# Kernel tuning notes

Hardware: AMD Instinct MI355X
Metric: run time of the kernel (lower is better)

Reference implementation:

```python
import jax, jax.numpy as jnp
import numpy as np

C = 32
N = 10000
E = 100000
LAT = 128
EPS = 1e-8
SQ3 = 3.0 ** 0.5
AVG_NEIGH = 10.0


def _sh2(p):
    # real l=2 spherical harmonics with principal axis = y (e3nn convention), m = -2..2
    x, y, z = p[..., 0], p[..., 1], p[..., 2]
    return jnp.stack([SQ3 * z * x, SQ3 * x * y, 0.5 * (3.0 * y * y - 1.0),
                      SQ3 * y * z, 0.5 * SQ3 * (z * z - x * x)], axis=-1)

# fixed sample points -> pseudoinverse for fitting Wigner-D at l=2: Y2(R p) = Y2(p) @ D2^T
_np_rng = np.random.default_rng(0)
_X = _np_rng.normal(size=(16, 3))
_X = _X / np.linalg.norm(_X, axis=1, keepdims=True)
_Xj = jnp.asarray(_X, jnp.float32)
_P2 = jnp.asarray(np.linalg.pinv(np.asarray(_sh2(jnp.asarray(_X, jnp.float32)))), jnp.float32)


def _wigner(vec):
    # per-edge rotation R with R @ n = e_y (edge aligned to y axis, e3nn convention)
    n = vec / jnp.clip(jnp.linalg.norm(vec, axis=-1, keepdims=True), 1e-9)
    ex = jnp.array([1.0, 0.0, 0.0], n.dtype)
    ez = jnp.array([0.0, 0.0, 1.0], n.dtype)
    a = jnp.where(jnp.abs(n[:, :1]) < 0.9, ex, ez)
    u = a - jnp.sum(a * n, axis=-1, keepdims=True) * n
    u = u / jnp.clip(jnp.linalg.norm(u, axis=-1, keepdims=True), 1e-9)
    v = jnp.cross(u, n)
    D1 = jnp.stack([u, n, v], axis=1)  # (E,3,3); Wigner-D for l=1 in (x,y,z) basis
    pts = jnp.einsum('eij,kj->eki', D1, _Xj)  # rotated sample points (E,K,3)
    D2 = jnp.swapaxes(jnp.einsum('mk,ekn->emn', _P2, _sh2(pts)), 1, 2)  # (E,5,5)
    return D1, D2


def _split(x):
    # flat [C x 0e | C x 1e | C x 2e] -> (.,C), (.,C,3), (.,C,5)
    return x[:, :C], x[:, C:4 * C].reshape(-1, C, 3), x[:, 4 * C:].reshape(-1, C, 5)


def _sln(x0, x1, x2, g0, b0, g1, g2):
    # separable layer norm: LN on scalars, degree-balanced RMS on l>0
    mu = jnp.mean(x0, axis=-1, keepdims=True)
    var = jnp.mean((x0 - mu) ** 2, axis=-1, keepdims=True)
    x0 = (x0 - mu) * jax.lax.rsqrt(var + EPS) * g0 + b0
    v = 0.5 * (jnp.mean(x1 ** 2, axis=(1, 2)) + jnp.mean(x2 ** 2, axis=(1, 2)))
    s = jax.lax.rsqrt(v + EPS)[:, None, None]
    return x0, x1 * s * g1[None, :, None], x2 * s * g2[None, :, None]


def _forward(latents, node_features, edge_features, edge_vector,
             g0n, b0n, g1n, g2n, g0e, b0e, g1e, g2e,
             w0s, w01, w02, wr1_1, wi1_1, wr1_2, wi1_2, wr2_2, wi2_2,
             wp0, bp0, wp1, wp2, w_env, b_env,
             atom_type, edge_index, active_edges):
    n0, n1, n2 = _sln(*_split(node_features), g0n, b0n, g1n, g2n)
    e0, e1, e2 = _sln(*_split(edge_features), g0e, b0e, g1e, g2e)
    ctr = edge_index[0][active_edges]
    nbr = edge_index[1][active_edges]
    vec = edge_vector[active_edges]
    lat = latents[active_edges]
    D1, D2 = _wigner(vec)
    # gather + concat: center | edge | neighbor, 3C channels per degree
    x0 = jnp.concatenate([n0[ctr], e0[active_edges], n0[nbr]], axis=1)
    x1 = jnp.concatenate([n1[ctr], e1[active_edges], n1[nbr]], axis=1)
    x2 = jnp.concatenate([n2[ctr], e2[active_edges], n2[nbr]], axis=1)
    # rotate into edge frame
    x1 = jnp.einsum('emn,ecn->ecm', D1, x1)
    x2 = jnp.einsum('emn,ecn->ecm', D2, x2)
    # SO2 linear (block structure over m about the edge axis = y; m index = l+m)
    s0 = 1.0 / jnp.sqrt(jnp.float32(9 * C))
    s1 = 1.0 / jnp.sqrt(jnp.float32(6 * C))
    s2 = 1.0 / jnp.sqrt(jnp.float32(3 * C))
    in0 = jnp.concatenate([x0, x1[:, :, 1], x2[:, :, 2]], axis=1)  # (E,9C) m=0
    y0 = in0 @ w0s.T * s0      # (E,3C): C scalars + 2C gates
    y1_0 = in0 @ w01.T * s0
    y2_0 = in0 @ w02.T * s0
    xp1 = jnp.concatenate([x1[:, :, 2], x2[:, :, 3]], axis=1)  # m=+1
    xm1 = jnp.concatenate([x1[:, :, 0], x2[:, :, 1]], axis=1)  # m=-1
    y1_p = (xp1 @ wr1_1.T - xm1 @ wi1_1.T) * s1
    y1_m = (xp1 @ wi1_1.T + xm1 @ wr1_1.T) * s1
    y2_p1 = (xp1 @ wr1_2.T - xm1 @ wi1_2.T) * s1
    y2_m1 = (xp1 @ wi1_2.T + xm1 @ wr1_2.T) * s1
    xp2 = x2[:, :, 4]
    xm2 = x2[:, :, 0]
    y2_p2 = (xp2 @ wr2_2.T - xm2 @ wi2_2.T) * s2
    y2_m2 = (xp2 @ wi2_2.T + xm2 @ wr2_2.T) * s2
    y1 = jnp.stack([y1_m, y1_0, y1_p], axis=-1)                      # (E,C,3)
    y2 = jnp.stack([y2_m2, y2_m1, y2_0, y2_p1, y2_p2], axis=-1)      # (E,C,5)
    # rotate back to global frame
    y1 = jnp.einsum('enm,ecn->ecm', D1, y1)
    y2 = jnp.einsum('enm,ecn->ecm', D2, y2)
    # Gate activation
    scal = jax.nn.silu(y0[:, :C])
    gate1 = jax.nn.sigmoid(y0[:, C:2 * C])
    gate2 = jax.nn.sigmoid(y0[:, 2 * C:])
    m1 = y1 * gate1[:, :, None]
    m2 = y2 * gate2[:, :, None]
    # lin_post (e3nn Linear, per-degree, bias on scalars)
    sc = 1.0 / jnp.sqrt(jnp.float32(C))
    m0 = scal @ wp0.T * sc + bp0
    m1 = jnp.einsum('dc,ecm->edm', wp1, m1) * sc
    m2 = jnp.einsum('dc,ecm->edm', wp2, m2) * sc
    # env weighting: per-irrep elementwise scalars from latents
    w = lat @ w_env.T * (1.0 / jnp.sqrt(jnp.float32(LAT))) + b_env
    m0 = m0 * w[:, :C]
    m1 = m1 * w[:, C:2 * C][:, :, None]
    m2 = m2 * w[:, 2 * C:][:, :, None]
    msg = jnp.concatenate([m0, m1.reshape(-1, 3 * C), m2.reshape(-1, 5 * C)], axis=1)
    agg = jax.ops.segment_sum(msg, ctr, num_segments=N) * (1.0 / jnp.sqrt(AVG_NEIGH))
    # residual update with logit-0 coefficient
    cu = 0.5
    c_old = 1.0 / jnp.sqrt(1.0 + cu * cu)
    c_new = cu * c_old
    return c_old * node_features + c_new * agg


def setup_inputs() -> dict:
    key = jax.random.key(0)
    ks = jax.random.split(key, 32)
    f = lambda i, shape: jax.random.normal(ks[i], shape, dtype=jnp.float32)
    return {
        'latents': f(0, (E, LAT)),
        'node_features': f(1, (N, 9 * C)),
        'edge_features': f(2, (E, 9 * C)),
        'edge_vector': f(3, (E, 3)),
        'atom_type': jax.random.randint(ks[4], (N,), 0, 10),
        'edge_index': jax.random.randint(ks[5], (2, E), 0, N),
        'active_edges': jnp.arange(E),
        'g0n': 1.0 + 0.1 * f(6, (C,)), 'b0n': 0.1 * f(7, (C,)),
        'g1n': 1.0 + 0.1 * f(8, (C,)), 'g2n': 1.0 + 0.1 * f(9, (C,)),
        'g0e': 1.0 + 0.1 * f(10, (C,)), 'b0e': 0.1 * f(11, (C,)),
        'g1e': 1.0 + 0.1 * f(12, (C,)), 'g2e': 1.0 + 0.1 * f(13, (C,)),
        'w0s': f(14, (3 * C, 9 * C)), 'w01': f(15, (C, 9 * C)), 'w02': f(16, (C, 9 * C)),
        'wr1_1': f(17, (C, 6 * C)), 'wi1_1': f(18, (C, 6 * C)),
        'wr1_2': f(19, (C, 6 * C)), 'wi1_2': f(20, (C, 6 * C)),
        'wr2_2': f(21, (C, 3 * C)), 'wi2_2': f(22, (C, 3 * C)),
        'wp0': f(23, (C, C)), 'bp0': 0.1 * f(24, (C,)),
        'wp1': f(25, (C, C)), 'wp2': f(26, (C, C)),
        'w_env': f(27, (3 * C, LAT)), 'b_env': 1.0 + 0.1 * f(28, (3 * C,)),
    }


def reference(latents, node_features, edge_features, edge_vector,
              g0n, b0n, g1n, g2n, g0e, b0e, g1e, g2e,
              w0s, w01, w02, wr1_1, wi1_1, wr1_2, wi1_2, wr2_2, wi2_2,
              wp0, bp0, wp1, wp2, w_env, b_env,
              atom_type, edge_index, active_edges):
    return _forward(latents, node_features, edge_features, edge_vector,
                    g0n, b0n, g1n, g2n, g0e, b0e, g1e, g2e,
                    w0s, w01, w02, wr1_1, wi1_1, wr1_2, wi1_2, wr2_2, wi2_2,
                    wp0, bp0, wp1, wp2, w_env, b_env,
                    atom_type, edge_index, active_edges)
```

## Files before the change

### kernel.cpp

```cpp
#include <hip/hip_runtime.h>
#include <hip/hip_bf16.h>
#include <math.h>

#define NN 10000
#define EE 100000
#define EPB 16
#define AST 1000
#define YSTH 456
#define PSTA 40
#define PSTP 36
#define MST 296
#define STG0 10368

#define SEG0 0
#define SEGP1 288
#define SEGM1 480
#define SEGP2 672
#define SEGM2 768
#define SEGL 864

#define Y0o   0
#define Y10o  96
#define Y20o  128
#define Y1Po  160
#define Y1Mo  192
#define Y2P1o 224
#define Y2M1o 256
#define Y2P2o 288
#define Y2M2o 320
#define WENVo 352

#define PK1 0
#define PK2 46080
#define PK3 95232
#define PK4 107520
#define PKP 119808
#define PKTOT 122880

#define WS_NRM 0
#define WS_PK  11520000
#define WS_CNT 11765760
#define WS_OFF 11831296
#define WS_CUR 11896832
#define WS_EL  11962368
#define WS_MSG 12486656
#define WS_REQ (WS_MSG + (size_t)EE*288*2)

#define SQ3F  1.7320508075688772f
#define S0F   0.05892556509887896f
#define S1F   0.07216878364870323f
#define S2F   0.10206207261596575f
#define SEF   0.08838834764831845f
#define SCF   0.17677669529663687f
#define COLDF 0.8944271909999159f
#define COEFF 0.1414213562373095f

typedef __attribute__((ext_vector_type(8))) short bf16x8;
typedef __attribute__((ext_vector_type(4))) float f32x4;

__device__ __forceinline__ ushort f2bf(float f) {
    __hip_bfloat16 h = __float2bfloat16(f);
    return __builtin_bit_cast(unsigned short, h);
}
__device__ __forceinline__ float bf2f(ushort u) {
    union { unsigned u; float f; } v; v.u = (unsigned)u << 16; return v.f;
}
__device__ __forceinline__ float fsig(float x) {
    return __builtin_amdgcn_rcpf(1.f + __expf(-x));
}

__device__ __forceinline__ int planar(int k) {
    if (k < 32) return k;
    if (k < 128) { int c = (k - 32) / 3, m = (k - 32) % 3; return 32 + 32*m + c; }
    int c = (k - 128) / 5, m = (k - 128) % 5; return 128 + 32*m + c;
}

__global__ __launch_bounds__(256) void pack_k(
    const float* __restrict__ w0s, const float* __restrict__ w01, const float* __restrict__ w02,
    const float* __restrict__ wr11, const float* __restrict__ wi11,
    const float* __restrict__ wr12, const float* __restrict__ wi12,
    const float* __restrict__ wr22, const float* __restrict__ wi22,
    const float* __restrict__ wenv,
    const float* __restrict__ wp0, const float* __restrict__ wp1, const float* __restrict__ wp2,
    ushort* __restrict__ pk)
{
    int i = blockIdx.x * 256 + threadIdx.x;
    if (i >= PKTOT) return;
    float val;
    if (i < PK2) {
        int idx = i - PK1;
        int tile = idx / 4608, rem = idx % 4608;
        int chunk = rem / 512, rem2 = rem % 512;
        int lane = rem2 / 8, j = rem2 % 8;
        int col = tile * 16 + (lane & 15);
        int k = chunk * 32 + (lane >> 4) * 8 + j;
        if (col < 96)       val = w0s[col * 288 + k];
        else if (col < 128) val = w01[(col - 96) * 288 + k];
        else                val = w02[(col - 128) * 288 + k];
    } else if (i < PK3) {
        int idx = i - PK2;
        int tile = idx / 6144, rem = idx % 6144;
        int chunk = rem / 512, rem2 = rem % 512;
        int lane = rem2 / 8, j = rem2 % 8;
        int col = tile * 16 + (lane & 15);
        int k = chunk * 32 + (lane >> 4) * 8 + j;
        int grp = col >> 5, c = col & 31;
        if (k < 192) {
            val = (grp == 0) ? wr11[c*192 + k] : (grp == 1) ? wi11[c*192 + k]
                : (grp == 2) ? wr12[c*192 + k] : wi12[c*192 + k];
        } else {
            int kk = k - 192;
            val = (grp == 0) ? -wi11[c*192 + kk] : (grp == 1) ? wr11[c*192 + kk]
                : (grp == 2) ? -wi12[c*192 + kk] : wr12[c*192 + kk];
        }
    } else if (i < PK4) {
        int idx = i - PK3;
        int tile = idx / 3072, rem = idx % 3072;
        int chunk = rem / 512, rem2 = rem % 512;
        int lane = rem2 / 8, j = rem2 % 8;
        int col = tile * 16 + (lane & 15);
        int k = chunk * 32 + (lane >> 4) * 8 + j;
        int grp = col >> 5, c = col & 31;
        if (k < 96) val = grp ? wi22[c*96 + k] : wr22[c*96 + k];
        else        val = grp ? wr22[c*96 + k - 96] : -wi22[c*96 + k - 96];
    } else if (i < PKP) {
        int idx = i - PK4;
        int tile = idx / 2048, rem = idx % 2048;
        int chunk = rem / 512, rem2 = rem % 512;
        int lane = rem2 / 8, j = rem2 % 8;
        int col = tile * 16 + (lane & 15);
        int k = chunk * 32 + (lane >> 4) * 8 + j;
        val = wenv[col * 128 + k];
    } else {
        int idx = i - PKP;
        int wpi = idx / 1024, rem = idx % 1024;
        int ct = rem / 512, rem2 = rem % 512;
        int lane = rem2 / 8, j = rem2 % 8;
        int col = ct * 16 + (lane & 15);
        int k = (lane >> 4) * 8 + j;
        const float* w = (wpi == 0) ? wp0 : (wpi == 1) ? wp1 : wp2;
        val = w[col * 32 + k];
    }
    pk[i] = f2bf(val);
}

__global__ __launch_bounds__(256) void node_norm_k(
    const float* __restrict__ nf,
    const float* __restrict__ g0, const float* __restrict__ b0,
    const float* __restrict__ g1, const float* __restrict__ g2,
    float* __restrict__ nrm, float* __restrict__ out)
{
    int row = blockIdx.x * 4 + (threadIdx.x >> 6);
    if (row >= NN) return;
    int lane = threadIdx.x & 63;
    const float* r = nf + (size_t)row * 288;
    float v0 = r[lane];
    float v1 = r[lane + 64];
    float v2 = r[lane + 128];
    float v3 = r[lane + 192];
    float v4 = (lane < 32) ? r[lane + 256] : 0.f;
    float s0 = 0.f, s0q = 0.f, q1 = 0.f, q2 = 0.f;
    if (lane < 32) { s0 = v0; s0q = v0*v0; } else { q1 = v0*v0; }
    q1 += v1*v1;
    q2 += v2*v2 + v3*v3 + v4*v4;
#pragma unroll
    for (int m = 1; m < 64; m <<= 1) {
        s0  += __shfl_xor(s0, m);
        s0q += __shfl_xor(s0q, m);
        q1  += __shfl_xor(q1, m);
        q2  += __shfl_xor(q2, m);
    }
    float mu  = s0 * (1.f/32.f);
    float var = s0q * (1.f/32.f) - mu*mu;
    float rs0 = rsqrtf(var + 1e-8f);
    float rv  = 0.5f * (q1 * (1.f/96.f) + q2 * (1.f/160.f));
    float rs  = rsqrtf(rv + 1e-8f);
    float* nr = nrm + (size_t)row * 288;
    {
        float res;
        if (lane < 32) res = (v0 - mu) * rs0 * g0[lane] + b0[lane];
        else { int c = (lane - 32) / 3; res = v0 * rs * g1[c]; }
        nr[planar(lane)] = res;
    }
    { int k = lane + 64;  int c = (k - 32) / 3;  nr[planar(k)] = v1 * rs * g1[c]; }
    { int k = lane + 128; int c = (k - 128) / 5; nr[planar(k)] = v2 * rs * g2[c]; }
    { int k = lane + 192; int c = (k - 128) / 5; nr[planar(k)] = v3 * rs * g2[c]; }
    if (lane < 32) { int k = lane + 256; int c = (k - 128) / 5; nr[planar(k)] = v4 * rs * g2[c]; }
    if (out) {
        float* orow = out + (size_t)row * 288;
        orow[lane]       = COLDF * v0;
        orow[lane + 64]  = COLDF * v1;
        orow[lane + 128] = COLDF * v2;
        orow[lane + 192] = COLDF * v3;
        if (lane < 32) orow[lane + 256] = COLDF * v4;
    }
}

__global__ __launch_bounds__(256) void zero_k(int* __restrict__ counts) {
    int i = blockIdx.x * 256 + threadIdx.x;
    if (i < NN) counts[i] = 0;
}
__global__ __launch_bounds__(256) void hist_k(
    const int* __restrict__ eidx, const int* __restrict__ act, int* __restrict__ counts) {
    int e = blockIdx.x * 256 + threadIdx.x;
    if (e >= EE) return;
    atomicAdd(&counts[eidx[act[e]]], 1);
}
__global__ __launch_bounds__(256) void scan_k(
    const int* __restrict__ counts, int* __restrict__ offs, int* __restrict__ curs) {
    __shared__ int sbuf[256];
    __shared__ int scarry;
    if (threadIdx.x == 0) scarry = 0;
    __syncthreads();
    for (int base = 0; base < NN; base += 256) {
        int i = base + threadIdx.x;
        int v = (i < NN) ? counts[i] : 0;
        sbuf[threadIdx.x] = v;
        __syncthreads();
        for (int off = 1; off < 256; off <<= 1) {
            int t = (threadIdx.x >= off) ? sbuf[threadIdx.x - off] : 0;
            __syncthreads();
            sbuf[threadIdx.x] += t;
            __syncthreads();
        }
        int excl = sbuf[threadIdx.x] - v;
        if (i < NN) { int o = scarry + excl; offs[i] = o; curs[i] = o; }
        __syncthreads();
        if (threadIdx.x == 255) scarry += sbuf[255];
        __syncthreads();
    }
}
__global__ __launch_bounds__(256) void scatter_k(
    const int* __restrict__ eidx, const int* __restrict__ act,
    int* __restrict__ curs, int* __restrict__ eslot) {
    int e = blockIdx.x * 256 + threadIdx.x;
    if (e >= EE) return;
    int pos = atomicAdd(&curs[eidx[act[e]]], 1);
    eslot[e] = pos;
}

__global__ __launch_bounds__(256) void gather_k(
    const ushort* __restrict__ msg, const int* __restrict__ offs,
    const int* __restrict__ counts,
    const float* __restrict__ nf, float* __restrict__ out)
{
    int node = blockIdx.x * 4 + (threadIdx.x >> 6);
    if (node >= NN) return;
    int lane = threadIdx.x & 63;
    int start = offs[node], cnt = counts[node];
    float a0 = 0.f, a1 = 0.f, a2 = 0.f, a3 = 0.f, a4 = 0.f;
    const ushort* mr = msg + (size_t)start * 288;
    for (int i = 0; i < cnt; ++i, mr += 288) {
        a0 += bf2f(mr[lane]);
        a1 += bf2f(mr[lane + 64]);
        a2 += bf2f(mr[lane + 128]);
        a3 += bf2f(mr[lane + 192]);
        if (lane < 32) a4 += bf2f(mr[lane + 256]);
    }
    const float* r = nf + (size_t)node * 288;
    float* o = out + (size_t)node * 288;
    o[lane]       = COLDF * r[lane]       + COEFF * a0;
    o[lane + 64]  = COLDF * r[lane + 64]  + COEFF * a1;
    o[lane + 128] = COLDF * r[lane + 128] + COEFF * a2;
    o[lane + 192] = COLDF * r[lane + 192] + COEFF * a3;
    if (lane < 32) o[lane + 256] = COLDF * r[lane + 256] + COEFF * a4;
}

__global__ __launch_bounds__(512, 6) void edge_k(
    const float* __restrict__ lat, const float* __restrict__ ef,
    const float* __restrict__ evec,
    const int* __restrict__ eidx, const int* __restrict__ act,
    const int* __restrict__ eslot,
    const float* __restrict__ g0e, const float* __restrict__ b0e,
    const float* __restrict__ g1e, const float* __restrict__ g2e,
    const ushort* __restrict__ pk,
    const float* __restrict__ bp0, const float* __restrict__ benv,
    const float* __restrict__ nrm, ushort* __restrict__ msg, float* __restrict__ out)
{
    __shared__ __align__(16) ushort sA[EPB * AST];
    __shared__ __align__(16) ushort sY[EPB * YSTH];
    __shared__ float sD1[EPB][12];
    __shared__ float sD2[EPB][28];
    __shared__ int sAe[EPB], sCtr[EPB], sNbr[EPB], sSlot[EPB];

    const int tid = threadIdx.x;
    const int wv = tid >> 6, lane = tid & 63;

    if (tid < EPB) {
        int ae = act[blockIdx.x * EPB + tid];
        sAe[tid] = ae;
        sCtr[tid] = eidx[ae];
        sNbr[tid] = eidx[EE + ae];
        sSlot[tid] = eslot ? eslot[blockIdx.x * EPB + tid] : 0;

        float vx = evec[3*ae], vy = evec[3*ae+1], vz = evec[3*ae+2];
        float nnv = fmaxf(sqrtf(vx*vx + vy*vy + vz*vz), 1e-9f);
        float nx = vx/nnv, ny = vy/nnv, nz = vz/nnv;
        float ax, az;
        if (fabsf(nx) < 0.9f) { ax = 1.f; az = 0.f; } else { ax = 0.f; az = 1.f; }
        float adn = ax*nx + az*nz;
        float ux = ax - adn*nx, uy = -adn*ny, uz = az - adn*nz;
        float un = fmaxf(sqrtf(ux*ux + uy*uy + uz*uz), 1e-9f);
        ux /= un; uy /= un; uz /= un;
        float wx = uy*nz - uz*ny, wy = uz*nx - ux*nz, wz = ux*ny - uy*nx;

        sD1[tid][0] = ux; sD1[tid][1] = uy; sD1[tid][2] = uz;
        sD1[tid][3] = nx; sD1[tid][4] = ny; sD1[tid][5] = nz;
        sD1[tid][6] = wx; sD1[tid][7] = wy; sD1[tid][8] = wz;

        float d2[5][5];
        d2[0][0] = wz*ux + uz*wx;  d2[0][1] = wx*uy + ux*wy;  d2[0][2] = SQ3F*wy*uy;
        d2[0][3] = wy*uz + uy*wz;  d2[0][4] = wz*uz - wx*ux;
        d2[1][0] = uz*nx + nz*ux;  d2[1][1] = ux*ny + nx*uy;  d2[1][2] = SQ3F*uy*ny;
        d2[1][3] = uy*nz + ny*uz;  d2[1][4] = uz*nz - ux*nx;
        d2[2][0] = SQ3F*nz*nx;     d2[2][1] = SQ3F*nx*ny;     d2[2][2] = 1.5f*ny*ny - 0.5f;
        d2[2][3] = SQ3F*ny*nz;     d2[2][4] = 0.5f*SQ3F*(nz*nz - nx*nx);
        d2[3][0] = nz*wx + wz*nx;  d2[3][1] = nx*wy + wx*ny;  d2[3][2] = SQ3F*ny*wy;
        d2[3][3] = ny*wz + wy*nz;  d2[3][4] = nz*wz - nx*wx;
        d2[4][0] = wz*wx - uz*ux;  d2[4][1] = wx*wy - ux*uy;  d2[4][2] = 0.5f*SQ3F*(wy*wy - uy*uy);
        d2[4][3] = wy*wz - uy*uz;  d2[4][4] = 0.5f*(wz*wz - uz*uz - wx*wx + ux*ux);
#pragma unroll
        for (int n = 0; n < 5; ++n)
#pragma unroll
            for (int m = 0; m < 5; ++m) sD2[tid][5*n + m] = d2[n][m];
    }
    __syncthreads();

    for (int it = 0; it < 2; ++it) {
        const int e = it * 8 + wv;
        const int ae = sAe[e];
        const int ctr = sCtr[e], nbr = sNbr[e];
        ushort* row = sA + e * AST;
        ushort* sEb = sY + e * YSTH;
        const float* efr = ef + (size_t)ae * 288;

        float ev0 = efr[lane];
        float ev1 = efr[lane + 64];
        float ev2 = efr[lane + 128];
        float ev3 = efr[lane + 192];
        float ev4 = (lane < 32) ? efr[lane + 256] : 0.f;
        float s0 = 0.f, s0q = 0.f, q1 = 0.f, q2 = 0.f;
        if (lane < 32) { s0 = ev0; s0q = ev0*ev0; } else { q1 = ev0*ev0; }
        q1 += ev1*ev1;
        q2 += ev2*ev2 + ev3*ev3 + ev4*ev4;
#pragma unroll
        for (int m = 1; m < 64; m <<= 1) {
            s0  += __shfl_xor(s0, m);
            s0q += __shfl_xor(s0q, m);
            q1  += __shfl_xor(q1, m);
            q2  += __shfl_xor(q2, m);
        }
        float mu  = s0 * (1.f/32.f);
        float rs0 = rsqrtf(s0q*(1.f/32.f) - mu*mu + 1e-8f);
        float rs  = rsqrtf(0.5f*(q1*(1.f/96.f) + q2*(1.f/160.f)) + 1e-8f);

        if (lane >= 32) { int c = (lane-32)/3, m = (lane-32)%3; sEb[32 + 32*m + c] = f2bf(ev0 * rs * g1e[c]); }
        { int k = lane+64;  int c = (k-32)/3,  m = (k-32)%3;  sEb[32 + 32*m + c]  = f2bf(ev1 * rs * g1e[c]); }
        { int k = lane+128; int c = (k-128)/5, m = (k-128)%5; sEb[128 + 32*m + c] = f2bf(ev2 * rs * g2e[c]); }
        { int k = lane+192; int c = (k-128)/5, m = (k-128)%5; sEb[128 + 32*m + c] = f2bf(ev3 * rs * g2e[c]); }
        if (lane < 32) { int k = lane+256; int c = (k-128)/5, m = (k-128)%5; sEb[128 + 32*m + c] = f2bf(ev4 * rs * g2e[c]); }

        if (lane < 32) {
            row[SEG0 + 32 + lane] = f2bf((ev0 - mu) * rs0 * g0e[lane] + b0e[lane]);
            row[SEG0 + lane]      = f2bf(nrm[(size_t)ctr*288 + lane]);
            row[SEG0 + 64 + lane] = f2bf(nrm[(size_t)nbr*288 + lane]);
        }
        {
            const float* lr = lat + (size_t)ae * 128;
            row[SEGL + lane]      = f2bf(lr[lane]);
            row[SEGL + 64 + lane] = f2bf(lr[lane + 64]);
        }
    }
    __syncthreads();

    {
        const int re = tid >> 5;
        const int rc = tid & 31;
        const float* bc = nrm + (size_t)sCtr[re] * 288;
        const float* bn = nrm + (size_t)sNbr[re] * 288;
        float c1v[3], c2v[5], n1v[3], n2v[5];
#pragma unroll
        for (int m = 0; m < 3; ++m) { c1v[m] = bc[32 + 32*m + rc]; n1v[m] = bn[32 + 32*m + rc]; }
#pragma unroll
        for (int m = 0; m < 5; ++m) { c2v[m] = bc[128 + 32*m + rc]; n2v[m] = bn[128 + 32*m + rc]; }
        float D1r[9], d2l[25];
#pragma unroll
        for (int i = 0; i < 9; ++i) D1r[i] = sD1[re][i];
#pragma unroll
        for (int i = 0; i < 25; ++i) d2l[i] = sD2[re][i];
        ushort* row = sA + re * AST;
        const ushort* sEb = sY + re * YSTH;
        float e1v[3], e2v[5];
#pragma unroll
        for (int m = 0; m < 3; ++m) e1v[m] = bf2f(sEb[32 + 32*m + rc]);
#pragma unroll
        for (int m = 0; m < 5; ++m) e2v[m] = bf2f(sEb[128 + 32*m + rc]);
#pragma unroll
        for (int p = 0; p < 3; ++p) {
            const int cc = rc + 32 * p;
            float x1v[3], x2v[5];
#pragma unroll
            for (int m = 0; m < 3; ++m) x1v[m] = (p == 0) ? c1v[m] : (p == 1) ? e1v[m] : n1v[m];
#pragma unroll
            for (int m = 0; m < 5; ++m) x2v[m] = (p == 0) ? c2v[m] : (p == 1) ? e2v[m] : n2v[m];
            float r0 = D1r[0]*x1v[0] + D1r[1]*x1v[1] + D1r[2]*x1v[2];
            float r1 = D1r[3]*x1v[0] + D1r[4]*x1v[1] + D1r[5]*x1v[2];
            float r2 = D1r[6]*x1v[0] + D1r[7]*x1v[1] + D1r[8]*x1v[2];
            float t[5];
#pragma unroll
            for (int m = 0; m < 5; ++m)
                t[m] = d2l[5*m+0]*x2v[0] + d2l[5*m+1]*x2v[1] + d2l[5*m+2]*x2v[2]
                     + d2l[5*m+3]*x2v[3] + d2l[5*m+4]*x2v[4];
            row[SEG0 + 96  + cc] = f2bf(r1);
            row[SEG0 + 192 + cc] = f2bf(t[2]);
            row[SEGP1 + cc]      = f2bf(r2);
            row[SEGP1 + 96 + cc] = f2bf(t[3]);
            row[SEGM1 + cc]      = f2bf(r0);
            row[SEGM1 + 96 + cc] = f2bf(t[1]);
            row[SEGP2 + cc]      = f2bf(t[4]);
            row[SEGM2 + cc]      = f2bf(t[0]);
        }
    }
    __syncthreads();

    for (int t = wv; t < 28; t += 8) {
        int kbase, nch, yoff, pbase; float scale;
        if (t < 10)      { kbase = SEG0;  nch = 9;  yoff = t*16;          scale = S0F; pbase = PK1 + t*9*512; }
        else if (t < 18) { kbase = SEGP1; nch = 12; yoff = 160+(t-10)*16; scale = S1F; pbase = PK2 + (t-10)*12*512; }
        else if (t < 22) { kbase = SEGP2; nch = 6;  yoff = 288+(t-18)*16; scale = S2F; pbase = PK3 + (t-18)*6*512; }
        else             { kbase = SEGL;  nch = 4;  yoff = 352+(t-22)*16; scale = SEF; pbase = PK4 + (t-22)*4*512; }
        f32x4 acc = {0.f, 0.f, 0.f, 0.f};
        const ushort* pa = sA + (lane & 15) * AST + kbase + (lane >> 4) * 8;
        const ushort* pb = pk + pbase + lane * 8;
        for (int ch = 0; ch < nch; ++ch) {
            bf16x8 a = *reinterpret_cast<const bf16x8*>(pa + ch * 32);
            bf16x8 b = *reinterpret_cast<const bf16x8*>(pb + ch * 512);
            acc = __builtin_amdgcn_mfma_f32_16x16x32_bf16(a, b, acc, 0, 0, 0);
        }
        const int col = yoff + (lane & 15);
        const int r0 = (lane >> 4) * 4;
        float bv = (t >= 22) ? benv[col - 352] : 0.f;
#pragma unroll
        for (int j = 0; j < 4; ++j)
            sY[(r0 + j) * YSTH + col] = f2bf(acc[j] * scale + bv);
    }
    __syncthreads();

    const int e2 = tid & 15, c = tid >> 4;
    const ushort* yrow = sY + e2 * YSTH;
    {
        float y0v = bf2f(yrow[Y0o + c]);
        float scv = y0v * fsig(y0v);
        float gg1 = fsig(bf2f(yrow[Y0o + 32 + c]));
        float gg2 = fsig(bf2f(yrow[Y0o + 64 + c]));
        sA[(0   + e2)*PSTA + c] = f2bf(scv);
        sA[(16  + e2)*PSTA + c] = f2bf(bf2f(yrow[Y1Mo  + c]) * gg1);
        sA[(32  + e2)*PSTA + c] = f2bf(bf2f(yrow[Y10o  + c]) * gg1);
        sA[(48  + e2)*PSTA + c] = f2bf(bf2f(yrow[Y1Po  + c]) * gg1);
        sA[(64  + e2)*PSTA + c] = f2bf(bf2f(yrow[Y2M2o + c]) * gg2);
        sA[(80  + e2)*PSTA + c] = f2bf(bf2f(yrow[Y2M1o + c]) * gg2);
        sA[(96  + e2)*PSTA + c] = f2bf(bf2f(yrow[Y20o  + c]) * gg2);
        sA[(112 + e2)*PSTA + c] = f2bf(bf2f(yrow[Y2P1o + c]) * gg2);
        sA[(128 + e2)*PSTA + c] = f2bf(bf2f(yrow[Y2P2o + c]) * gg2);
    }
    __syncthreads();

    f32x4 pacc[3];
#pragma unroll
    for (int q = 0; q < 3; ++q) {
        const int t = wv + 8*q;
        if (t < 18) {
            const int rt = t >> 1, ct = t & 1;
            const int wpi = (rt == 0) ? 0 : (rt < 4) ? 1 : 2;
            bf16x8 a = *reinterpret_cast<const bf16x8*>(sA + (rt*16 + (lane & 15))*PSTA + (lane >> 4)*8);
            bf16x8 b = *reinterpret_cast<const bf16x8*>(pk + PKP + wpi*1024 + ct*512 + lane*8);
            f32x4 z = {0.f, 0.f, 0.f, 0.f};
            pacc[q] = __builtin_amdgcn_mfma_f32_16x16x32_bf16(a, b, z, 0, 0, 0);
        }
    }
    __syncthreads();

    float* sPf = reinterpret_cast<float*>(sA);
#pragma unroll
    for (int q = 0; q < 3; ++q) {
        const int t = wv + 8*q;
        if (t < 18) {
            const int rt = t >> 1, ct = t & 1;
            const int col = ct*16 + (lane & 15);
#pragma unroll
            for (int j = 0; j < 4; ++j) {
                const int rw = rt*16 + (lane >> 4)*4 + j;
                sPf[rw*PSTP + col] = pacc[q][j];
            }
        }
    }
    __syncthreads();

    const int d = c;
    {
        float wv0g = bf2f(yrow[WENVo + d]);
        float m0v = (sPf[e2*PSTP + d] * SCF + bp0[d]) * wv0g;

        float p1v[3], p2v[5];
#pragma unroll
        for (int m = 0; m < 3; ++m) p1v[m] = sPf[(16 + 16*m + e2)*PSTP + d];
#pragma unroll
        for (int m = 0; m < 5; ++m) p2v[m] = sPf[(64 + 16*m + e2)*PSTP + d];

        float wv1g = bf2f(yrow[WENVo + 32 + d]) * SCF;
        float wv2g = bf2f(yrow[WENVo + 64 + d]) * SCF;

        float o1[3], o2[5];
#pragma unroll
        for (int mm = 0; mm < 3; ++mm)
            o1[mm] = (sD1[e2][mm]*p1v[0] + sD1[e2][3+mm]*p1v[1] + sD1[e2][6+mm]*p1v[2]) * wv1g;
#pragma unroll
        for (int mm = 0; mm < 5; ++mm)
            o2[mm] = (sD2[e2][mm]*p2v[0] + sD2[e2][5+mm]*p2v[1] + sD2[e2][10+mm]*p2v[2]
                    + sD2[e2][15+mm]*p2v[3] + sD2[e2][20+mm]*p2v[4]) * wv2g;

        if (msg) {
            ushort* stg = sA + STG0 + e2 * MST;
            stg[d] = f2bf(m0v);
#pragma unroll
            for (int mm = 0; mm < 3; ++mm) stg[32 + 3*d + mm] = f2bf(o1[mm]);
#pragma unroll
            for (int mm = 0; mm < 5; ++mm) stg[128 + 5*d + mm] = f2bf(o2[mm]);
        } else {
            float* ob = out + (size_t)sCtr[e2] * 288;
            atomicAdd(ob + d, COEFF * m0v);
#pragma unroll
            for (int mm = 0; mm < 3; ++mm) atomicAdd(ob + 32 + 3*d + mm, COEFF * o1[mm]);
#pragma unroll
            for (int mm = 0; mm < 5; ++mm) atomicAdd(ob + 128 + 5*d + mm, COEFF * o2[mm]);
        }
    }
    __syncthreads();

    if (msg) {
        const int e = tid >> 5, j = tid & 31;
        const ushort* src = sA + STG0 + e * MST;
        ushort* dst = msg + (size_t)sSlot[e] * 288;
        *reinterpret_cast<bf16x8*>(dst + j*8) = *reinterpret_cast<const bf16x8*>(src + j*8);
        if (j < 4)
            *reinterpret_cast<bf16x8*>(dst + (j+32)*8) = *reinterpret_cast<const bf16x8*>(src + (j+32)*8);
    }
}

extern "C" void kernel_launch(void* const* d_in, const int* in_sizes, int n_in,
                              void* d_out, int out_size, void* d_ws, size_t ws_size,
                              hipStream_t stream)
{
    const float* latents = (const float*)d_in[0];
    const float* nf      = (const float*)d_in[1];
    const float* efe     = (const float*)d_in[2];
    const float* evec    = (const float*)d_in[3];
    const int*   eidx    = (const int*)d_in[5];
    const int*   act     = (const int*)d_in[6];
    const float* g0n = (const float*)d_in[7];
    const float* b0n = (const float*)d_in[8];
    const float* g1n = (const float*)d_in[9];
    const float* g2n = (const float*)d_in[10];
    const float* g0e = (const float*)d_in[11];
    const float* b0e = (const float*)d_in[12];
    const float* g1e = (const float*)d_in[13];
    const float* g2e = (const float*)d_in[14];
    const float* w0s = (const float*)d_in[15];
    const float* w01 = (const float*)d_in[16];
    const float* w02 = (const float*)d_in[17];
    const float* wr11 = (const float*)d_in[18];
    const float* wi11 = (const float*)d_in[19];
    const float* wr12 = (const float*)d_in[20];
    const float* wi12 = (const float*)d_in[21];
    const float* wr22 = (const float*)d_in[22];
    const float* wi22 = (const float*)d_in[23];
    const float* wp0 = (const float*)d_in[24];
    const float* bp0 = (const float*)d_in[25];
    const float* wp1 = (const float*)d_in[26];
    const float* wp2 = (const float*)d_in[27];
    const float* wenv = (const float*)d_in[28];
    const float* benv = (const float*)d_in[29];
    float* out = (float*)d_out;

    char* ws = (char*)d_ws;
    float* nrm  = (float*)(ws + WS_NRM);
    ushort* pkw = (ushort*)(ws + WS_PK);
    const bool use_msg = (ws_size >= WS_REQ);
    int* counts = (int*)(ws + WS_CNT);
    int* offs   = (int*)(ws + WS_OFF);
    int* curs   = (int*)(ws + WS_CUR);
    int* eslot  = (int*)(ws + WS_EL);
    ushort* msg = (ushort*)(ws + WS_MSG);

    pack_k<<<(PKTOT + 255) / 256, 256, 0, stream>>>(w0s, w01, w02, wr11, wi11, wr12, wi12,
                                                    wr22, wi22, wenv, wp0, wp1, wp2, pkw);
    node_norm_k<<<(NN + 3) / 4, 256, 0, stream>>>(nf, g0n, b0n, g1n, g2n, nrm,
                                                  use_msg ? nullptr : out);
    if (use_msg) {
        zero_k<<<(NN + 255) / 256, 256, 0, stream>>>(counts);
        hist_k<<<(EE + 255) / 256, 256, 0, stream>>>(eidx, act, counts);
        scan_k<<<1, 256, 0, stream>>>(counts, offs, curs);
        scatter_k<<<(EE + 255) / 256, 256, 0, stream>>>(eidx, act, curs, eslot);
    }
    edge_k<<<EE / EPB, 512, 0, stream>>>(latents, efe, evec, eidx, act,
        use_msg ? eslot : nullptr,
        g0e, b0e, g1e, g2e, pkw, bp0, benv, nrm, use_msg ? msg : nullptr, out);
    if (use_msg) {
        gather_k<<<(NN + 3) / 4, 256, 0, stream>>>(msg, offs, counts, nf, out);
    }
}
```

Before: 285.3 us.

## Fuse setup kernels, rewrite scan, shrink edge kernel LDS with swizzled reuse

```diff
diff --git a/kernel.cpp b/kernel.cpp
--- a/kernel.cpp
+++ b/kernel.cpp
@@ -5,12 +5,8 @@
 #define NN 10000
 #define EE 100000
 #define EPB 16
-#define AST 1000
-#define YSTH 456
-#define PSTA 40
-#define PSTP 36
-#define MST 296
-#define STG0 10368
+#define AST 992
+#define PA0 480
 
 #define SEG0 0
 #define SEGP1 288
@@ -55,6 +51,10 @@
 #define COLDF 0.8944271909999159f
 #define COEFF 0.1414213562373095f
 
+#define NNB 2500
+#define PKB ((PKTOT + 255) / 256)
+#define HSB ((EE + 255) / 256)
+
 typedef __attribute__((ext_vector_type(8))) short bf16x8;
 typedef __attribute__((ext_vector_type(4))) float f32x4;
 
@@ -68,168 +68,172 @@
 __device__ __forceinline__ float fsig(float x) {
     return __builtin_amdgcn_rcpf(1.f + __expf(-x));
 }
-
 __device__ __forceinline__ int planar(int k) {
     if (k < 32) return k;
     if (k < 128) { int c = (k - 32) / 3, m = (k - 32) % 3; return 32 + 32*m + c; }
     int c = (k - 128) / 5, m = (k - 128) % 5; return 128 + 32*m + c;
 }
 
-__global__ __launch_bounds__(256) void pack_k(
+__global__ __launch_bounds__(256) void init_k(
+    const float* __restrict__ nf,
+    const float* __restrict__ g0, const float* __restrict__ b0,
+    const float* __restrict__ g1, const float* __restrict__ g2,
+    float* __restrict__ nrm, float* __restrict__ out,
     const float* __restrict__ w0s, const float* __restrict__ w01, const float* __restrict__ w02,
     const float* __restrict__ wr11, const float* __restrict__ wi11,
     const float* __restrict__ wr12, const float* __restrict__ wi12,
     const float* __restrict__ wr22, const float* __restrict__ wi22,
     const float* __restrict__ wenv,
     const float* __restrict__ wp0, const float* __restrict__ wp1, const float* __restrict__ wp2,
-    ushort* __restrict__ pk)
+    ushort* __restrict__ pk,
+    const int* __restrict__ eidx, const int* __restrict__ act, int* __restrict__ counts)
 {
-    int i = blockIdx.x * 256 + threadIdx.x;
-    if (i >= PKTOT) return;
-    float val;
-    if (i < PK2) {
-        int idx = i - PK1;
-        int tile = idx / 4608, rem = idx % 4608;
-        int chunk = rem / 512, rem2 = rem % 512;
-        int lane = rem2 / 8, j = rem2 % 8;
-        int col = tile * 16 + (lane & 15);
-        int k = chunk * 32 + (lane >> 4) * 8 + j;
-        if (col < 96)       val = w0s[col * 288 + k];
-        else if (col < 128) val = w01[(col - 96) * 288 + k];
-        else                val = w02[(col - 128) * 288 + k];
-    } else if (i < PK3) {
-        int idx = i - PK2;
-        int tile = idx / 6144, rem = idx % 6144;
-        int chunk = rem / 512, rem2 = rem % 512;
-        int lane = rem2 / 8, j = rem2 % 8;
-        int col = tile * 16 + (lane & 15);
-        int k = chunk * 32 + (lane >> 4) * 8 + j;
-        int grp = col >> 5, c = col & 31;
-        if (k < 192) {
-            val = (grp == 0) ? wr11[c*192 + k] : (grp == 1) ? wi11[c*192 + k]
-                : (grp == 2) ? wr12[c*192 + k] : wi12[c*192 + k];
+    const int bid = blockIdx.x;
+    if (bid < NNB) {
+        int row = bid * 4 + (threadIdx.x >> 6);
+        if (row >= NN) return;
+        int lane = threadIdx.x & 63;
+        const float* r = nf + (size_t)row * 288;
+        float v0 = r[lane];
+        float v1 = r[lane + 64];
+        float v2 = r[lane + 128];
+        float v3 = r[lane + 192];
+        float v4 = (lane < 32) ? r[lane + 256] : 0.f;
+        float s0 = 0.f, s0q = 0.f, q1 = 0.f, q2 = 0.f;
+        if (lane < 32) { s0 = v0; s0q = v0*v0; } else { q1 = v0*v0; }
+        q1 += v1*v1;
+        q2 += v2*v2 + v3*v3 + v4*v4;
+#pragma unroll
+        for (int m = 1; m < 64; m <<= 1) {
+            s0  += __shfl_xor(s0, m);
+            s0q += __shfl_xor(s0q, m);
+            q1  += __shfl_xor(q1, m);
+            q2  += __shfl_xor(q2, m);
+        }
+        float mu  = s0 * (1.f/32.f);
+        float rs0 = rsqrtf(s0q*(1.f/32.f) - mu*mu + 1e-8f);
+        float rs  = rsqrtf(0.5f*(q1*(1.f/96.f) + q2*(1.f/160.f)) + 1e-8f);
+        float* nr = nrm + (size_t)row * 288;
+        {
+            float res;
+            if (lane < 32) res = (v0 - mu) * rs0 * g0[lane] + b0[lane];
+            else { int c = (lane - 32) / 3; res = v0 * rs * g1[c]; }
+            nr[planar(lane)] = res;
+        }
+        { int k = lane + 64;  int c = (k - 32) / 3;  nr[planar(k)] = v1 * rs * g1[c]; }
+        { int k = lane + 128; int c = (k - 128) / 5; nr[planar(k)] = v2 * rs * g2[c]; }
+        { int k = lane + 192; int c = (k - 128) / 5; nr[planar(k)] = v3 * rs * g2[c]; }
+        if (lane < 32) { int k = lane + 256; int c = (k - 128) / 5; nr[planar(k)] = v4 * rs * g2[c]; }
+        if (out) {
+            float* orow = out + (size_t)row * 288;
+            orow[lane]       = COLDF * v0;
+            orow[lane + 64]  = COLDF * v1;
+            orow[lane + 128] = COLDF * v2;
+            orow[lane + 192] = COLDF * v3;
+            if (lane < 32) orow[lane + 256] = COLDF * v4;
+        }
+    } else if (bid < NNB + PKB) {
+        int i = (bid - NNB) * 256 + threadIdx.x;
+        if (i >= PKTOT) return;
+        float val;
+        if (i < PK2) {
+            int idx = i - PK1;
+            int tile = idx / 4608, rem = idx % 4608;
+            int chunk = rem / 512, rem2 = rem % 512;
+            int lane = rem2 / 8, j = rem2 % 8;
+            int col = tile * 16 + (lane & 15);
+            int k = chunk * 32 + (lane >> 4) * 8 + j;
+            if (col < 96)       val = w0s[col * 288 + k];
+            else if (col < 128) val = w01[(col - 96) * 288 + k];
+            else                val = w02[(col - 128) * 288 + k];
+        } else if (i < PK3) {
+            int idx = i - PK2;
+            int tile = idx / 6144, rem = idx % 6144;
+            int chunk = rem / 512, rem2 = rem % 512;
+            int lane = rem2 / 8, j = rem2 % 8;
+            int col = tile * 16 + (lane & 15);
+            int k = chunk * 32 + (lane >> 4) * 8 + j;
+            int grp = col >> 5, c = col & 31;
+            if (k < 192) {
+                val = (grp == 0) ? wr11[c*192 + k] : (grp == 1) ? wi11[c*192 + k]
+                    : (grp == 2) ? wr12[c*192 + k] : wi12[c*192 + k];
+            } else {
+                int kk = k - 192;
+                val = (grp == 0) ? -wi11[c*192 + kk] : (grp == 1) ? wr11[c*192 + kk]
+                    : (grp == 2) ? -wi12[c*192 + kk] : wr12[c*192 + kk];
+            }
+        } else if (i < PK4) {
+            int idx = i - PK3;
+            int tile = idx / 3072, rem = idx % 3072;
+            int chunk = rem / 512, rem2 = rem % 512;
+            int lane = rem2 / 8, j = rem2 % 8;
+            int col = tile * 16 + (lane & 15);
+            int k = chunk * 32 + (lane >> 4) * 8 + j;
+            int grp = col >> 5, c = col & 31;
+            if (k < 96) val = grp ? wi22[c*96 + k] : wr22[c*96 + k];
+            else        val = grp ? wr22[c*96 + k - 96] : -wi22[c*96 + k - 96];
+        } else if (i < PKP) {
+            int idx = i - PK4;
+            int tile = idx / 2048, rem = idx % 2048;
+            int chunk = rem / 512, rem2 = rem % 512;
+            int lane = rem2 / 8, j = rem2 % 8;
+            int col = tile * 16 + (lane & 15);
+            int k = chunk * 32 + (lane >> 4) * 8 + j;
+            val = wenv[col * 128 + k];
         } else {
-            int kk = k - 192;
-            val = (grp == 0) ? -wi11[c*192 + kk] : (grp == 1) ? wr11[c*192 + kk]
-                : (grp == 2) ? -wi12[c*192 + kk] : wr12[c*192 + kk];
-        }
-    } else if (i < PK4) {
-        int idx = i - PK3;
-        int tile = idx / 3072, rem = idx % 3072;
-        int chunk = rem / 512, rem2 = rem % 512;
-        int lane = rem2 / 8, j = rem2 % 8;
-        int col = tile * 16 + (lane & 15);
-        int k = chunk * 32 + (lane >> 4) * 8 + j;
-        int grp = col >> 5, c = col & 31;
-        if (k < 96) val = grp ? wi22[c*96 + k] : wr22[c*96 + k];
-        else        val = grp ? wr22[c*96 + k - 96] : -wi22[c*96 + k - 96];
-    } else if (i < PKP) {
-        int idx = i - PK4;
-        int tile = idx / 2048, rem = idx % 2048;
-        int chunk = rem / 512, rem2 = rem % 512;
-        int lane = rem2 / 8, j = rem2 % 8;
-        int col = tile * 16 + (lane & 15);
-        int k = chunk * 32 + (lane >> 4) * 8 + j;
-        val = wenv[col * 128 + k];
+            int idx = i - PKP;
+            int wpi = idx / 1024, rem = idx % 1024;
+            int ct = rem / 512, rem2 = rem % 512;
+            int lane = rem2 / 8, j = rem2 % 8;
+            int col = ct * 16 + (lane & 15);
+            int k = (lane >> 4) * 8 + j;
+            const float* w = (wpi == 0) ? wp0 : (wpi == 1) ? wp1 : wp2;
+            val = w[col * 32 + k];
+        }
+        pk[i] = f2bf(val);
     } else {
-        int idx = i - PKP;
-        int wpi = idx / 1024, rem = idx % 1024;
-        int ct = rem / 512, rem2 = rem % 512;
-        int lane = rem2 / 8, j = rem2 % 8;
-        int col = ct * 16 + (lane & 15);
-        int k = (lane >> 4) * 8 + j;
-        const float* w = (wpi == 0) ? wp0 : (wpi == 1) ? wp1 : wp2;
-        val = w[col * 32 + k];
-    }
-    pk[i] = f2bf(val);
-}
-
-__global__ __launch_bounds__(256) void node_norm_k(
-    const float* __restrict__ nf,
-    const float* __restrict__ g0, const float* __restrict__ b0,
-    const float* __restrict__ g1, const float* __restrict__ g2,
-    float* __restrict__ nrm, float* __restrict__ out)
+        int e = (bid - NNB - PKB) * 256 + threadIdx.x;
+        if (e >= EE) return;
+        atomicAdd(&counts[eidx[act[e]]], 1);
+    }
+}
+
+__global__ __launch_bounds__(1024) void scan_k(
+    const int* __restrict__ counts, int* __restrict__ offs, int* __restrict__ curs)
 {
-    int row = blockIdx.x * 4 + (threadIdx.x >> 6);
-    if (row >= NN) return;
-    int lane = threadIdx.x & 63;
-    const float* r = nf + (size_t)row * 288;
-    float v0 = r[lane];
-    float v1 = r[lane + 64];
-    float v2 = r[lane + 128];
-    float v3 = r[lane + 192];
-    float v4 = (lane < 32) ? r[lane + 256] : 0.f;
-    float s0 = 0.f, s0q = 0.f, q1 = 0.f, q2 = 0.f;
-    if (lane < 32) { s0 = v0; s0q = v0*v0; } else { q1 = v0*v0; }
-    q1 += v1*v1;
-    q2 += v2*v2 + v3*v3 + v4*v4;
-#pragma unroll
-    for (int m = 1; m < 64; m <<= 1) {
-        s0  += __shfl_xor(s0, m);
-        s0q += __shfl_xor(s0q, m);
-        q1  += __shfl_xor(q1, m);
-        q2  += __shfl_xor(q2, m);
-    }
-    float mu  = s0 * (1.f/32.f);
-    float var = s0q * (1.f/32.f) - mu*mu;
-    float rs0 = rsqrtf(var + 1e-8f);
-    float rv  = 0.5f * (q1 * (1.f/96.f) + q2 * (1.f/160.f));
-    float rs  = rsqrtf(rv + 1e-8f);
-    float* nr = nrm + (size_t)row * 288;
-    {
-        float res;
-        if (lane < 32) res = (v0 - mu) * rs0 * g0[lane] + b0[lane];
-        else { int c = (lane - 32) / 3; res = v0 * rs * g1[c]; }
-        nr[planar(lane)] = res;
-    }
-    { int k = lane + 64;  int c = (k - 32) / 3;  nr[planar(k)] = v1 * rs * g1[c]; }
-    { int k = lane + 128; int c = (k - 128) / 5; nr[planar(k)] = v2 * rs * g2[c]; }
-    { int k = lane + 192; int c = (k - 128) / 5; nr[planar(k)] = v3 * rs * g2[c]; }
-    if (lane < 32) { int k = lane + 256; int c = (k - 128) / 5; nr[planar(k)] = v4 * rs * g2[c]; }
-    if (out) {
-        float* orow = out + (size_t)row * 288;
-        orow[lane]       = COLDF * v0;
-        orow[lane + 64]  = COLDF * v1;
-        orow[lane + 128] = COLDF * v2;
-        orow[lane + 192] = COLDF * v3;
-        if (lane < 32) orow[lane + 256] = COLDF * v4;
-    }
-}
-
-__global__ __launch_bounds__(256) void zero_k(int* __restrict__ counts) {
-    int i = blockIdx.x * 256 + threadIdx.x;
-    if (i < NN) counts[i] = 0;
-}
-__global__ __launch_bounds__(256) void hist_k(
-    const int* __restrict__ eidx, const int* __restrict__ act, int* __restrict__ counts) {
-    int e = blockIdx.x * 256 + threadIdx.x;
-    if (e >= EE) return;
-    atomicAdd(&counts[eidx[act[e]]], 1);
-}
-__global__ __launch_bounds__(256) void scan_k(
-    const int* __restrict__ counts, int* __restrict__ offs, int* __restrict__ curs) {
-    __shared__ int sbuf[256];
-    __shared__ int scarry;
-    if (threadIdx.x == 0) scarry = 0;
-    __syncthreads();
-    for (int base = 0; base < NN; base += 256) {
-        int i = base + threadIdx.x;
-        int v = (i < NN) ? counts[i] : 0;
-        sbuf[threadIdx.x] = v;
-        __syncthreads();
-        for (int off = 1; off < 256; off <<= 1) {
-            int t = (threadIdx.x >= off) ? sbuf[threadIdx.x - off] : 0;
-            __syncthreads();
-            sbuf[threadIdx.x] += t;
-            __syncthreads();
-        }
-        int excl = sbuf[threadIdx.x] - v;
-        if (i < NN) { int o = scarry + excl; offs[i] = o; curs[i] = o; }
-        __syncthreads();
-        if (threadIdx.x == 255) scarry += sbuf[255];
-        __syncthreads();
-    }
-}
+    const int tid = threadIdx.x;
+    const int base = tid * 10;
+    int v[10]; int s = 0;
+#pragma unroll
+    for (int j = 0; j < 10; ++j) {
+        int i = base + j;
+        int c = (i < NN) ? counts[i] : 0;
+        v[j] = s; s += c;
+    }
+    const int lane = tid & 63, wv = tid >> 6;
+    int inc = s;
+#pragma unroll
+    for (int off = 1; off < 64; off <<= 1) {
+        int t = __shfl_up(inc, off);
+        if (lane >= off) inc += t;
+    }
+    __shared__ int wsum[16], wbase[16];
+    if (lane == 63) wsum[wv] = inc;
+    __syncthreads();
+    if (tid == 0) {
+        int acc = 0;
+#pragma unroll
+        for (int i = 0; i < 16; ++i) { int t = wsum[i]; wbase[i] = acc; acc += t; }
+    }
+    __syncthreads();
+    const int texcl = wbase[wv] + inc - s;
+#pragma unroll
+    for (int j = 0; j < 10; ++j) {
+        int i = base + j;
+        if (i < NN) { int o = texcl + v[j]; offs[i] = o; curs[i] = o; }
+    }
+}
+
 __global__ __launch_bounds__(256) void scatter_k(
     const int* __restrict__ eidx, const int* __restrict__ act,
     int* __restrict__ curs, int* __restrict__ eslot) {
@@ -248,25 +252,30 @@
     if (node >= NN) return;
     int lane = threadIdx.x & 63;
     int start = offs[node], cnt = counts[node];
-    float a0 = 0.f, a1 = 0.f, a2 = 0.f, a3 = 0.f, a4 = 0.f;
-    const ushort* mr = msg + (size_t)start * 288;
-    for (int i = 0; i < cnt; ++i, mr += 288) {
-        a0 += bf2f(mr[lane]);
-        a1 += bf2f(mr[lane + 64]);
-        a2 += bf2f(mr[lane + 128]);
-        a3 += bf2f(mr[lane + 192]);
-        if (lane < 32) a4 += bf2f(mr[lane + 256]);
-    }
-    const float* r = nf + (size_t)node * 288;
-    float* o = out + (size_t)node * 288;
-    o[lane]       = COLDF * r[lane]       + COEFF * a0;
-    o[lane + 64]  = COLDF * r[lane + 64]  + COEFF * a1;
-    o[lane + 128] = COLDF * r[lane + 128] + COEFF * a2;
-    o[lane + 192] = COLDF * r[lane + 192] + COEFF * a3;
-    if (lane < 32) o[lane + 256] = COLDF * r[lane + 256] + COEFF * a4;
-}
-
-__global__ __launch_bounds__(512, 6) void edge_k(
+    float a0x = 0.f, a0y = 0.f, a1x = 0.f, a1y = 0.f, a2x = 0.f, a2y = 0.f;
+    const uint* mu = (const uint*)(msg + (size_t)start * 288);
+    for (int i = 0; i < cnt; ++i, mu += 144) {
+        uint u0 = mu[lane];
+        uint u1 = mu[lane + 64];
+        uint u2 = (lane < 16) ? mu[lane + 128] : 0u;
+        a0x += bf2f((ushort)u0); a0y += bf2f((ushort)(u0 >> 16));
+        a1x += bf2f((ushort)u1); a1y += bf2f((ushort)(u1 >> 16));
+        a2x += bf2f((ushort)u2); a2y += bf2f((ushort)(u2 >> 16));
+    }
+    const float2* r2 = (const float2*)(nf + (size_t)node * 288);
+    float2* o2 = (float2*)(out + (size_t)node * 288);
+    float2 r;
+    r = r2[lane];
+    o2[lane]      = make_float2(COLDF*r.x + COEFF*a0x, COLDF*r.y + COEFF*a0y);
+    r = r2[lane + 64];
+    o2[lane + 64] = make_float2(COLDF*r.x + COEFF*a1x, COLDF*r.y + COEFF*a1y);
+    if (lane < 16) {
+        r = r2[lane + 128];
+        o2[lane + 128] = make_float2(COLDF*r.x + COEFF*a2x, COLDF*r.y + COEFF*a2y);
+    }
+}
+
+__global__ __launch_bounds__(512, 8) void edge_k(
     const float* __restrict__ lat, const float* __restrict__ ef,
     const float* __restrict__ evec,
     const int* __restrict__ eidx, const int* __restrict__ act,
@@ -278,7 +287,6 @@
     const float* __restrict__ nrm, ushort* __restrict__ msg, float* __restrict__ out)
 {
     __shared__ __align__(16) ushort sA[EPB * AST];
-    __shared__ __align__(16) ushort sY[EPB * YSTH];
     __shared__ float sD1[EPB][12];
     __shared__ float sD2[EPB][28];
     __shared__ int sAe[EPB], sCtr[EPB], sNbr[EPB], sSlot[EPB];
@@ -331,7 +339,7 @@
         const int ae = sAe[e];
         const int ctr = sCtr[e], nbr = sNbr[e];
         ushort* row = sA + e * AST;
-        ushort* sEb = sY + e * YSTH;
+        ushort* rowEB = row + 64;
         const float* efr = ef + (size_t)ae * 288;
 
         float ev0 = efr[lane];
@@ -354,11 +362,11 @@
         float rs0 = rsqrtf(s0q*(1.f/32.f) - mu*mu + 1e-8f);
         float rs  = rsqrtf(0.5f*(q1*(1.f/96.f) + q2*(1.f/160.f)) + 1e-8f);
 
-        if (lane >= 32) { int c = (lane-32)/3, m = (lane-32)%3; sEb[32 + 32*m + c] = f2bf(ev0 * rs * g1e[c]); }
-        { int k = lane+64;  int c = (k-32)/3,  m = (k-32)%3;  sEb[32 + 32*m + c]  = f2bf(ev1 * rs * g1e[c]); }
-        { int k = lane+128; int c = (k-128)/5, m = (k-128)%5; sEb[128 + 32*m + c] = f2bf(ev2 * rs * g2e[c]); }
-        { int k = lane+192; int c = (k-128)/5, m = (k-128)%5; sEb[128 + 32*m + c] = f2bf(ev3 * rs * g2e[c]); }
-        if (lane < 32) { int k = lane+256; int c = (k-128)/5, m = (k-128)%5; sEb[128 + 32*m + c] = f2bf(ev4 * rs * g2e[c]); }
+        if (lane >= 32) { int c = (lane-32)/3, m = (lane-32)%3; rowEB[32 + 32*m + c] = f2bf(ev0 * rs * g1e[c]); }
+        { int k = lane+64;  int c = (k-32)/3,  m = (k-32)%3;  rowEB[32 + 32*m + c]  = f2bf(ev1 * rs * g1e[c]); }
+        { int k = lane+128; int c = (k-128)/5, m = (k-128)%5; rowEB[128 + 32*m + c] = f2bf(ev2 * rs * g2e[c]); }
+        { int k = lane+192; int c = (k-128)/5, m = (k-128)%5; rowEB[128 + 32*m + c] = f2bf(ev3 * rs * g2e[c]); }
+        if (lane < 32) { int k = lane+256; int c = (k-128)/5, m = (k-128)%5; rowEB[128 + 32*m + c] = f2bf(ev4 * rs * g2e[c]); }
 
         if (lane < 32) {
             row[SEG0 + 32 + lane] = f2bf((ev0 - mu) * rs0 * g0e[lane] + b0e[lane]);
@@ -383,18 +391,19 @@
         for (int m = 0; m < 3; ++m) { c1v[m] = bc[32 + 32*m + rc]; n1v[m] = bn[32 + 32*m + rc]; }
 #pragma unroll
         for (int m = 0; m < 5; ++m) { c2v[m] = bc[128 + 32*m + rc]; n2v[m] = bn[128 + 32*m + rc]; }
+        ushort* row = sA + re * AST;
+        const ushort* rowEB = row + 64;
+        float e1v[3], e2v[5];
+#pragma unroll
+        for (int m = 0; m < 3; ++m) e1v[m] = bf2f(rowEB[32 + 32*m + rc]);
+#pragma unroll
+        for (int m = 0; m < 5; ++m) e2v[m] = bf2f(rowEB[128 + 32*m + rc]);
+        asm volatile("" ::: "memory");
         float D1r[9], d2l[25];
 #pragma unroll
         for (int i = 0; i < 9; ++i) D1r[i] = sD1[re][i];
 #pragma unroll
         for (int i = 0; i < 25; ++i) d2l[i] = sD2[re][i];
-        ushort* row = sA + re * AST;
-        const ushort* sEb = sY + re * YSTH;
-        float e1v[3], e2v[5];
-#pragma unroll
-        for (int m = 0; m < 3; ++m) e1v[m] = bf2f(sEb[32 + 32*m + rc]);
-#pragma unroll
-        for (int m = 0; m < 5; ++m) e2v[m] = bf2f(sEb[128 + 32*m + rc]);
 #pragma unroll
         for (int p = 0; p < 3; ++p) {
             const int cc = rc + 32 * p;
@@ -423,64 +432,88 @@
     }
     __syncthreads();
 
-    for (int t = wv; t < 28; t += 8) {
-        int kbase, nch, yoff, pbase; float scale;
-        if (t < 10)      { kbase = SEG0;  nch = 9;  yoff = t*16;          scale = S0F; pbase = PK1 + t*9*512; }
-        else if (t < 18) { kbase = SEGP1; nch = 12; yoff = 160+(t-10)*16; scale = S1F; pbase = PK2 + (t-10)*12*512; }
-        else if (t < 22) { kbase = SEGP2; nch = 6;  yoff = 288+(t-18)*16; scale = S2F; pbase = PK3 + (t-18)*6*512; }
-        else             { kbase = SEGL;  nch = 4;  yoff = 352+(t-22)*16; scale = SEF; pbase = PK4 + (t-22)*4*512; }
-        f32x4 acc = {0.f, 0.f, 0.f, 0.f};
-        const ushort* pa = sA + (lane & 15) * AST + kbase + (lane >> 4) * 8;
-        const ushort* pb = pk + pbase + lane * 8;
-        for (int ch = 0; ch < nch; ++ch) {
-            bf16x8 a = *reinterpret_cast<const bf16x8*>(pa + ch * 32);
-            bf16x8 b = *reinterpret_cast<const bf16x8*>(pb + ch * 512);
-            acc = __builtin_amdgcn_mfma_f32_16x16x32_bf16(a, b, acc, 0, 0, 0);
-        }
-        const int col = yoff + (lane & 15);
-        const int r0 = (lane >> 4) * 4;
-        float bv = (t >= 22) ? benv[col - 352] : 0.f;
-#pragma unroll
-        for (int j = 0; j < 4; ++j)
-            sY[(r0 + j) * YSTH + col] = f2bf(acc[j] * scale + bv);
-    }
-    __syncthreads();
-
-    const int e2 = tid & 15, c = tid >> 4;
-    const ushort* yrow = sY + e2 * YSTH;
+    f32x4 pacc[4];
+#pragma unroll
+    for (int q = 0; q < 4; ++q) {
+        const int t = wv + 8*q;
+        if (t < 28) {
+            int kbase, nch, pbase; float scale;
+            if (t < 10)      { kbase = SEG0;  nch = 9;  scale = S0F; pbase = PK1 + t*9*512; }
+            else if (t < 18) { kbase = SEGP1; nch = 12; scale = S1F; pbase = PK2 + (t-10)*12*512; }
+            else if (t < 22) { kbase = SEGP2; nch = 6;  scale = S2F; pbase = PK3 + (t-18)*6*512; }
+            else             { kbase = SEGL;  nch = 4;  scale = SEF; pbase = PK4 + (t-22)*4*512; }
+            f32x4 acc = {0.f, 0.f, 0.f, 0.f};
+            const ushort* pa = sA + (lane & 15) * AST + kbase + (lane >> 4) * 8;
+            const ushort* pb = pk + pbase + lane * 8;
+            for (int ch = 0; ch < nch; ++ch) {
+                bf16x8 a = *reinterpret_cast<const bf16x8*>(pa + ch * 32);
+                bf16x8 b = *reinterpret_cast<const bf16x8*>(pb + ch * 512);
+                acc = __builtin_amdgcn_mfma_f32_16x16x32_bf16(a, b, acc, 0, 0, 0);
+            }
+            int yoff = (t < 10) ? t*16 : (t < 18) ? 160+(t-10)*16 : (t < 22) ? 288+(t-18)*16 : 352+(t-22)*16;
+            float bv = (t >= 22) ? benv[yoff + (lane & 15) - 352] : 0.f;
+#pragma unroll
+            for (int j = 0; j < 4; ++j) acc[j] = acc[j] * scale + bv;
+            pacc[q] = acc;
+        }
+    }
+    __syncthreads();
+
+#pragma unroll
+    for (int q = 0; q < 4; ++q) {
+        const int t = wv + 8*q;
+        if (t < 28) {
+            int yoff = (t < 10) ? t*16 : (t < 18) ? 160+(t-10)*16 : (t < 22) ? 288+(t-18)*16 : 352+(t-22)*16;
+            const int col = yoff + (lane & 15);
+            const int r0 = (lane >> 4) * 4;
+#pragma unroll
+            for (int j = 0; j < 4; ++j) {
+                const int rr = r0 + j;
+                sA[rr * AST + (col ^ (rr << 1))] = f2bf(pacc[q][j]);
+            }
+        }
+    }
+    __syncthreads();
+
+    const int e2 = tid & 15, d = tid >> 4;
     {
-        float y0v = bf2f(yrow[Y0o + c]);
+        const int rowb = e2 * AST;
+        const int sw = e2 << 1;
+        auto LDY = [&](int x) { return bf2f(sA[rowb + (x ^ sw)]); };
+        float y0v = LDY(Y0o + d);
         float scv = y0v * fsig(y0v);
-        float gg1 = fsig(bf2f(yrow[Y0o + 32 + c]));
-        float gg2 = fsig(bf2f(yrow[Y0o + 64 + c]));
-        sA[(0   + e2)*PSTA + c] = f2bf(scv);
-        sA[(16  + e2)*PSTA + c] = f2bf(bf2f(yrow[Y1Mo  + c]) * gg1);
-        sA[(32  + e2)*PSTA + c] = f2bf(bf2f(yrow[Y10o  + c]) * gg1);
-        sA[(48  + e2)*PSTA + c] = f2bf(bf2f(yrow[Y1Po  + c]) * gg1);
-        sA[(64  + e2)*PSTA + c] = f2bf(bf2f(yrow[Y2M2o + c]) * gg2);
-        sA[(80  + e2)*PSTA + c] = f2bf(bf2f(yrow[Y2M1o + c]) * gg2);
-        sA[(96  + e2)*PSTA + c] = f2bf(bf2f(yrow[Y20o  + c]) * gg2);
-        sA[(112 + e2)*PSTA + c] = f2bf(bf2f(yrow[Y2P1o + c]) * gg2);
-        sA[(128 + e2)*PSTA + c] = f2bf(bf2f(yrow[Y2P2o + c]) * gg2);
-    }
-    __syncthreads();
-
-    f32x4 pacc[3];
+        float gg1 = fsig(LDY(Y0o + 32 + d));
+        float gg2 = fsig(LDY(Y0o + 64 + d));
+        const int pabase = rowb + PA0 + 8*((d >> 3) ^ (e2 & 3)) + (d & 7);
+        sA[pabase + 0*56] = f2bf(scv);
+        sA[pabase + 1*56] = f2bf(LDY(Y1Mo  + d) * gg1);
+        sA[pabase + 2*56] = f2bf(LDY(Y10o  + d) * gg1);
+        sA[pabase + 3*56] = f2bf(LDY(Y1Po  + d) * gg1);
+        sA[pabase + 4*56] = f2bf(LDY(Y2M2o + d) * gg2);
+        sA[pabase + 5*56] = f2bf(LDY(Y2M1o + d) * gg2);
+        sA[pabase + 6*56] = f2bf(LDY(Y20o  + d) * gg2);
+        sA[pabase + 7*56] = f2bf(LDY(Y2P1o + d) * gg2);
+        sA[pabase + 8*56] = f2bf(LDY(Y2P2o + d) * gg2);
+    }
+    __syncthreads();
+
+    f32x4 pacc2[3];
 #pragma unroll
     for (int q = 0; q < 3; ++q) {
         const int t = wv + 8*q;
         if (t < 18) {
             const int rt = t >> 1, ct = t & 1;
             const int wpi = (rt == 0) ? 0 : (rt < 4) ? 1 : 2;
-            bf16x8 a = *reinterpret_cast<const bf16x8*>(sA + (rt*16 + (lane & 15))*PSTA + (lane >> 4)*8);
+            const int ar = lane & 15;
+            bf16x8 a = *reinterpret_cast<const bf16x8*>(
+                sA + ar*AST + PA0 + rt*56 + 8*((lane >> 4) ^ (ar & 3)));
             bf16x8 b = *reinterpret_cast<const bf16x8*>(pk + PKP + wpi*1024 + ct*512 + lane*8);
             f32x4 z = {0.f, 0.f, 0.f, 0.f};
-            pacc[q] = __builtin_amdgcn_mfma_f32_16x16x32_bf16(a, b, z, 0, 0, 0);
-        }
-    }
-    __syncthreads();
-
-    float* sPf = reinterpret_cast<float*>(sA);
+            pacc2[q] = __builtin_amdgcn_mfma_f32_16x16x32_bf16(a, b, z, 0, 0, 0);
+        }
+    }
+    __syncthreads();
+
 #pragma unroll
     for (int q = 0; q < 3; ++q) {
         const int t = wv + 8*q;
@@ -489,28 +522,34 @@
             const int col = ct*16 + (lane & 15);
 #pragma unroll
             for (int j = 0; j < 4; ++j) {
-                const int rw = rt*16 + (lane >> 4)*4 + j;
-                sPf[rw*PSTP + col] = pacc[q][j];
+                const int ee = (lane >> 4)*4 + j;
+                const int colSw = (col + 4*ee) & 31;
+                float* fp = reinterpret_cast<float*>(sA + ee * AST);
+                if (rt < 4) fp[rt*44 + colSw] = pacc2[q][j];
+                else        fp[240 + (rt-4)*50 + colSw] = pacc2[q][j];
             }
         }
     }
     __syncthreads();
 
-    const int d = c;
+    float m0v, o1[3], o2[5];
     {
-        float wv0g = bf2f(yrow[WENVo + d]);
-        float m0v = (sPf[e2*PSTP + d] * SCF + bp0[d]) * wv0g;
-
+        const int rowb = e2 * AST;
+        const int sw = e2 << 1;
+        auto LDY = [&](int x) { return bf2f(sA[rowb + (x ^ sw)]); };
+        const float* fp = reinterpret_cast<const float*>(sA + rowb);
+        const int cd = (d + 4*e2) & 31;
+        float p0 = fp[cd];
         float p1v[3], p2v[5];
 #pragma unroll
-        for (int m = 0; m < 3; ++m) p1v[m] = sPf[(16 + 16*m + e2)*PSTP + d];
-#pragma unroll
-        for (int m = 0; m < 5; ++m) p2v[m] = sPf[(64 + 16*m + e2)*PSTP + d];
-
-        float wv1g = bf2f(yrow[WENVo + 32 + d]) * SCF;
-        float wv2g = bf2f(yrow[WENVo + 64 + d]) * SCF;
-
-        float o1[3], o2[5];
+        for (int m = 0; m < 3; ++m) p1v[m] = fp[(1+m)*44 + cd];
+#pragma unroll
+        for (int m = 0; m < 5; ++m) p2v[m] = fp[240 + m*50 + cd];
+
+        float wv0g = LDY(WENVo + d);
+        float wv1g = LDY(WENVo + 32 + d) * SCF;
+        float wv2g = LDY(WENVo + 64 + d) * SCF;
+        m0v = (p0 * SCF + bp0[d]) * wv0g;
 #pragma unroll
         for (int mm = 0; mm < 3; ++mm)
             o1[mm] = (sD1[e2][mm]*p1v[0] + sD1[e2][3+mm]*p1v[1] + sD1[e2][6+mm]*p1v[2]) * wv1g;
@@ -518,32 +557,30 @@
         for (int mm = 0; mm < 5; ++mm)
             o2[mm] = (sD2[e2][mm]*p2v[0] + sD2[e2][5+mm]*p2v[1] + sD2[e2][10+mm]*p2v[2]
                     + sD2[e2][15+mm]*p2v[3] + sD2[e2][20+mm]*p2v[4]) * wv2g;
-
-        if (msg) {
-            ushort* stg = sA + STG0 + e2 * MST;
-            stg[d] = f2bf(m0v);
-#pragma unroll
-            for (int mm = 0; mm < 3; ++mm) stg[32 + 3*d + mm] = f2bf(o1[mm]);
-#pragma unroll
-            for (int mm = 0; mm < 5; ++mm) stg[128 + 5*d + mm] = f2bf(o2[mm]);
-        } else {
-            float* ob = out + (size_t)sCtr[e2] * 288;
-            atomicAdd(ob + d, COEFF * m0v);
-#pragma unroll
-            for (int mm = 0; mm < 3; ++mm) atomicAdd(ob + 32 + 3*d + mm, COEFF * o1[mm]);
-#pragma unroll
-            for (int mm = 0; mm < 5; ++mm) atomicAdd(ob + 128 + 5*d + mm, COEFF * o2[mm]);
-        }
-    }
-    __syncthreads();
+    }
 
     if (msg) {
+        __syncthreads();
+        ushort* stg = sA + e2 * AST;
+        stg[d] = f2bf(m0v);
+#pragma unroll
+        for (int mm = 0; mm < 3; ++mm) stg[32 + 3*d + mm] = f2bf(o1[mm]);
+#pragma unroll
+        for (int mm = 0; mm < 5; ++mm) stg[128 + 5*d + mm] = f2bf(o2[mm]);
+        __syncthreads();
         const int e = tid >> 5, j = tid & 31;
-        const ushort* src = sA + STG0 + e * MST;
+        const ushort* src = sA + e * AST;
         ushort* dst = msg + (size_t)sSlot[e] * 288;
         *reinterpret_cast<bf16x8*>(dst + j*8) = *reinterpret_cast<const bf16x8*>(src + j*8);
         if (j < 4)
-            *reinterpret_cast<bf16x8*>(dst + (j+32)*8) = *reinterpret_cast<const bf16x8*>(src + (j+32)*8);
+            *reinterpret_cast<bf16x8*>(dst + 256 + j*8) = *reinterpret_cast<const bf16x8*>(src + 256 + j*8);
+    } else {
+        float* ob = out + (size_t)sCtr[e2] * 288;
+        atomicAdd(ob + d, COEFF * m0v);
+#pragma unroll
+        for (int mm = 0; mm < 3; ++mm) atomicAdd(ob + 32 + 3*d + mm, COEFF * o1[mm]);
+#pragma unroll
+        for (int mm = 0; mm < 5; ++mm) atomicAdd(ob + 128 + 5*d + mm, COEFF * o2[mm]);
     }
 }
 
@@ -592,14 +629,13 @@
     int* eslot  = (int*)(ws + WS_EL);
     ushort* msg = (ushort*)(ws + WS_MSG);
 
-    pack_k<<<(PKTOT + 255) / 256, 256, 0, stream>>>(w0s, w01, w02, wr11, wi11, wr12, wi12,
-                                                    wr22, wi22, wenv, wp0, wp1, wp2, pkw);
-    node_norm_k<<<(NN + 3) / 4, 256, 0, stream>>>(nf, g0n, b0n, g1n, g2n, nrm,
-                                                  use_msg ? nullptr : out);
+    hipMemsetAsync(counts, 0, NN * sizeof(int), stream);
+    init_k<<<NNB + PKB + HSB, 256, 0, stream>>>(
+        nf, g0n, b0n, g1n, g2n, nrm, use_msg ? nullptr : out,
+        w0s, w01, w02, wr11, wi11, wr12, wi12, wr22, wi22, wenv, wp0, wp1, wp2, pkw,
+        eidx, act, counts);
     if (use_msg) {
-        zero_k<<<(NN + 255) / 256, 256, 0, stream>>>(counts);
-        hist_k<<<(EE + 255) / 256, 256, 0, stream>>>(eidx, act, counts);
-        scan_k<<<1, 256, 0, stream>>>(counts, offs, curs);
+        scan_k<<<1, 1024, 0, stream>>>(counts, offs, curs);
         scatter_k<<<(EE + 255) / 256, 256, 0, stream>>>(eidx, act, curs, eslot);
     }
     edge_k<<<EE / EPB, 512, 0, stream>>>(latents, efe, evec, eidx, act,
```

After: 232.1 us. 18.6% less time.
